# Optimization experiments

Hardware: AMD Instinct MI355X
Metric: run time of the kernel (lower is better)

## Reference

```python
import jax, jax.numpy as jnp
import numpy as np

B, T, I, H, L = 4096, 3, 16, 512, 8  # batch, seq (fixed=3 by fc1), input, hidden, layers


def setup_inputs() -> dict:
    key = jax.random.key(0)
    ks = jax.random.split(key, 12)
    s = 1.0 / np.sqrt(H)  # PyTorch LSTM init scale
    inp = {
        "x": jax.random.normal(ks[0], (B, T, I), dtype=jnp.float32),
        "W_ih0": jax.random.uniform(ks[1], (4 * H, I), jnp.float32, -s, s),
        "W_ih_rest": jax.random.uniform(ks[2], (L - 1, 4 * H, H), jnp.float32, -s, s),
        "W_hh": jax.random.uniform(ks[3], (L, 4 * H, H), jnp.float32, -s, s),
        "b_ih": jax.random.uniform(ks[4], (L, 4 * H), jnp.float32, -s, s),
        "b_hh": jax.random.uniform(ks[5], (L, 4 * H), jnp.float32, -s, s),
        "fc1_w": jax.random.uniform(ks[6], (64, H * T), jnp.float32, -1 / np.sqrt(H * T), 1 / np.sqrt(H * T)),
        "fc1_b": jax.random.uniform(ks[7], (64,), jnp.float32, -1 / np.sqrt(H * T), 1 / np.sqrt(H * T)),
        "fc2_w": jax.random.uniform(ks[8], (3, 64), jnp.float32, -1 / 8.0, 1 / 8.0),
        "fc2_b": jax.random.uniform(ks[9], (3,), jnp.float32, -1 / 8.0, 1 / 8.0),
    }
    return inp


def _lstm_layer(x_tbd, Wih, Whh, bih, bhh):
    # x_tbd: [T, B, D_in] -> [T, B, H]; PyTorch gate order i, f, g, o
    Bsz = x_tbd.shape[1]
    h0 = jnp.zeros((Bsz, H), x_tbd.dtype)
    c0 = jnp.zeros((Bsz, H), x_tbd.dtype)
    # precompute input projections for all timesteps in one matmul
    xg = jnp.einsum('tbd,gd->tbg', x_tbd, Wih) + (bih + bhh)

    def step(carry, xg_t):
        h, c = carry
        gates = xg_t + h @ Whh.T  # [B, 4H]
        i, f, g, o = jnp.split(gates, 4, axis=-1)
        i = jax.nn.sigmoid(i)
        f = jax.nn.sigmoid(f)
        g = jnp.tanh(g)
        o = jax.nn.sigmoid(o)
        c = f * c + i * g
        h = o * jnp.tanh(c)
        return (h, c), h

    _, hs = jax.lax.scan(step, (h0, c0), xg)
    return hs  # [T, B, H]


def reference(x, W_ih0, W_ih_rest, W_hh, b_ih, b_hh, fc1_w, fc1_b, fc2_w, fc2_b):
    h = jnp.transpose(x, (1, 0, 2))  # [T, B, I] (time-major for scan)
    for l in range(L):
        Wih = W_ih0 if l == 0 else W_ih_rest[l - 1]
        h = _lstm_layer(h, Wih, W_hh[l], b_ih[l], b_hh[l])
        # dropout between layers is inference-disabled (eval mode)
    out = jnp.transpose(h, (1, 0, 2)).reshape(x.shape[0], -1)  # [B, T*H]
    out = out @ fc1_w.T + fc1_b
    out = out @ fc2_w.T + fc2_b
    return out
```

## Files before the change

kernel.cpp:

```cpp
#include <hip/hip_runtime.h>
#include <hip/hip_bf16.h>
#include <math.h>


#define BATCH 4096
#define TT 3
#define HH 512
#define LL 8

typedef __attribute__((ext_vector_type(4))) int   i32x4;

#define S_W 0.04419417382f
#define GSCALE   (S_W / 16129.0f)
#define C_SCALE   8192.0f
#define C_INV     (1.0f / 8192.0f)

__device__ inline void gl_lds16(const void* g, void* l) {
    __builtin_amdgcn_global_load_lds(
        (const __attribute__((address_space(1))) void*)g,
        (__attribute__((address_space(3))) void*)l, 16, 0, 0);
}

__device__ inline float fsig(float x) {
    return __builtin_amdgcn_rcpf(1.f + __expf(-x));
}
__device__ inline float ftanh(float x) {
    const float e = __expf(-2.f * __builtin_fabsf(x));
    const float t = (1.f - e) * __builtin_amdgcn_rcpf(1.f + e);
    return __builtin_copysignf(t, x);
}


__global__ __launch_bounds__(256) void prep_w_i8(
    const float* __restrict__ Wihrest, const float* __restrict__ Whh,
    char* __restrict__ WihPh, char* __restrict__ WhhPh)
{
    const int e = blockIdx.x * 256 + threadIdx.x;
    const int mat = e >> 18;
    const int rem = e & 262143;
    const int row = rem >> 7;
    const int k4  = (rem & 127) << 2;
    const float* src; char *dh;
    if (mat < 7) {
        src = Wihrest + (size_t)mat * 1048576;
        dh = WihPh + (size_t)mat * 1048576;
    } else {
        const int l = mat - 7;
        src = Whh + (size_t)l * 1048576;
        dh = WhhPh + (size_t)l * 1048576;
    }
    const int q = row >> 9, j = row & 511;
    const int np = ((j >> 4) << 6) | (q << 4) | (j & 15);
    const int rw = np & 127;
    const int swz = ((rw >> 1) & 3) << 4;
    const size_t off = (size_t)(np >> 7) * 65536 + (size_t)(k4 >> 6) * 8192
                     + (size_t)rw * 64 + ((k4 & 63) ^ swz);
    const float4 v = *(const float4*)(src + (size_t)row * 512 + k4);
    const float inv = 127.0f / S_W;
    int i0 = __float2int_rn(v.x * inv); i0 = i0 > 127 ? 127 : (i0 < -127 ? -127 : i0);
    int i1 = __float2int_rn(v.y * inv); i1 = i1 > 127 ? 127 : (i1 < -127 ? -127 : i1);
    int i2 = __float2int_rn(v.z * inv); i2 = i2 > 127 ? 127 : (i2 < -127 ? -127 : i2);
    int i3 = __float2int_rn(v.w * inv); i3 = i3 > 127 ? 127 : (i3 < -127 ? -127 : i3);
    unsigned hw = (unsigned char)(signed char)i0 | ((unsigned char)(signed char)i1 << 8) |
                  ((unsigned char)(signed char)i2 << 16) | ((unsigned)(unsigned char)(signed char)i3 << 24);
    *(unsigned*)(dh + off) = hw;
}

__global__ __launch_bounds__(256) void prep_w0_i8(
    const float* __restrict__ W0, char* __restrict__ Dh)
{
    const int row = blockIdx.x * 256 + threadIdx.x;
    if (row >= 2048) return;
    const int q = row >> 9, j = row & 511;
    const int np = ((j >> 4) << 6) | (q << 4) | (j & 15);
    const int sl = (np >> 1) & 3;
    const size_t off = (size_t)(np >> 7) * 8192 + (size_t)(np & 127) * 64;
    const float inv = 127.0f / S_W;
    signed char bh[64];
#pragma unroll
    for (int k = 0; k < 16; ++k) {
        int iv = __float2int_rn(W0[(size_t)row * 16 + k] * inv);
        iv = iv > 127 ? 127 : (iv < -127 ? -127 : iv);
        bh[k] = (signed char)iv;
    }
#pragma unroll
    for (int k = 16; k < 64; ++k) bh[k] = 0;
#pragma unroll
    for (int i = 0; i < 4; ++i) {
        *(int4*)(Dh + off + (i ^ sl) * 16) = *(int4*)(bh + i * 16);
    }
}

__global__ __launch_bounds__(256) void prep_x_i8(
    const float* __restrict__ x, char* __restrict__ Xh)
{
    const int id = blockIdx.x * 256 + threadIdx.x;
    if (id >= TT * BATCH) return;
    const int t = id >> 12, b = id & 4095;
    const float* src = x + ((size_t)b * TT + t) * 16;
    const int sl = (b >> 1) & 3;
    const size_t off = (size_t)t * 262144 + (size_t)(b >> 7) * 8192 + (size_t)(b & 127) * 64;
    const float inv = 127.0f / 8.0f;
    signed char bh[64];
#pragma unroll
    for (int k = 0; k < 16; ++k) {
        int iv = __float2int_rn(src[k] * inv);
        iv = iv > 127 ? 127 : (iv < -127 ? -127 : iv);
        bh[k] = (signed char)iv;
    }
#pragma unroll
    for (int k = 16; k < 64; ++k) bh[k] = 0;
#pragma unroll
    for (int i = 0; i < 4; ++i) {
        *(int4*)(Xh + off + (i ^ sl) * 16) = *(int4*)(bh + i * 16);
    }
}

__global__ __launch_bounds__(256) void prep_bsum(
    const float* __restrict__ bih, const float* __restrict__ bhh, float* __restrict__ Bsum)
{
    const int id = blockIdx.x * 256 + threadIdx.x;
    if (id >= LL * 2048) return;
    const int l = id >> 11, row = id & 2047;
    const int q = row >> 9, j = row & 511;
    const int np = ((j >> 4) << 6) | (q << 4) | (j & 15);
    Bsum[(size_t)l * 2048 + np] = bih[(size_t)l * 2048 + row] + bhh[(size_t)l * 2048 + row];
}

__global__ __launch_bounds__(256) void prep_fc1t(
    const float* __restrict__ fc1w, float* __restrict__ fc1T)
{
    const int id = blockIdx.x * 256 + threadIdx.x;
    if (id >= 64 * 1536) return;
    const int m = id / 1536, k = id % 1536;
    fc1T[(size_t)k * 64 + m] = fc1w[id];
}


struct CellDesc {
    const char* A0h;
    const char* W0h;
    const char* A1h;
    const char* W1h;
    const float* bsum; const short* Cin;
    char* HoutH;
    short* Cout; float* Hf32;
    int nk0, aStr0, wStr0, shiftAmt;
};
struct DiagArgs { CellDesc c[3]; };

__global__ __launch_bounds__(512, 8) void lstm_diag(DiagArgs args)
{
    __shared__ char ldsA[2][8192];
    __shared__ char ldsB[3][8192];
    const int tid = threadIdx.x;
    const CellDesc d = args.c[blockIdx.x >> 9];
    const int inner = blockIdx.x & 511;
    const int xcd = inner & 7, q8 = inner >> 3;
    const int mrow = ((xcd & 3) << 3) | (q8 & 7);
    const int col  = ((xcd >> 2) << 3) | (q8 >> 3);
    const int m0 = mrow << 7;
    const int lane = tid & 63, wid = tid >> 6;
    const int wr = wid >> 1;
    const int wc = wid & 1;
    const int ln = lane & 15, lh = lane >> 4;
    const int sl = (ln >> 1) & 3;

    const int nkTot = d.nk0 + (d.A1h ? 8 : 0);
    const int start = (d.shiftAmt == 0) ? (((q8 & 3) * nkTot) >> 2) : 0;

    const int lhs = (lh ^ sl) << 4;
    const int aO0 = (((wr << 5) + (0 << 4) + ln) << 6) + lhs;
    const int aO1 = (((wr << 5) + (1 << 4) + ln) << 6) + lhs;
    const int bO0 = (((wc << 6) + (0 << 4) + ln) << 6) + lhs;
    const int bO1 = (((wc << 6) + (1 << 4) + ln) << 6) + lhs;
    const int bO2 = (((wc << 6) + (2 << 4) + ln) << 6) + lhs;
    const int bO3 = (((wc << 6) + (3 << 4) + ln) << 6) + lhs;

    i32x4 accM[2][4];
#pragma unroll
    for (int m = 0; m < 2; ++m)
#pragma unroll
        for (int n = 0; n < 4; ++n) accM[m][n] = (i32x4){0,0,0,0};

    auto stageA = [&](int ks, int buf) {
        const char *pA;
        if (ks < d.nk0) {
            pA = d.A0h + (size_t)mrow * d.aStr0 + (size_t)ks * 8192;
        } else {
            pA = d.A1h + (size_t)mrow * 65536 + (size_t)(ks - d.nk0) * 8192;
        }
        const int o = tid << 4;
        gl_lds16(pA + o, &ldsA[buf][0] + o);
    };
    auto stageB = [&](int ks, int buf) {
        const char *pB;
        if (ks < d.nk0) {
            pB = d.W0h + (size_t)col * d.wStr0 + (size_t)ks * 8192;
        } else {
            pB = d.W1h + (size_t)col * 65536 + (size_t)(ks - d.nk0) * 8192;
        }
        const int o = tid << 4;
        gl_lds16(pB + o, &ldsB[buf][0] + o);
    };
    auto ksAt = [&](int i) { int k = start + i; return (k >= nkTot) ? k - nkTot : k; };

    stageA(ksAt(0), 0);
    stageB(ksAt(0), 0);
    if (nkTot > 1) {
        stageB(ksAt(1), 1);
        asm volatile("s_waitcnt vmcnt(1)" ::: "memory");
    } else {
        asm volatile("s_waitcnt vmcnt(0)" ::: "memory");
    }
    __builtin_amdgcn_s_barrier();

    int bb = 0;
    for (int i = 0; i < nkTot; ++i) {
        const int ab = i & 1;
        if (i + 1 < nkTot) stageA(ksAt(i + 1), ab ^ 1);
        const bool haveB2 = (i + 2 < nkTot);
        if (haveB2) { int nb = bb + 2; if (nb >= 3) nb -= 3; stageB(ksAt(i + 2), nb); }

        const char* dA = &ldsA[ab][0];
        const char* dB = &ldsB[bb][0];
        i32x4 a_h[2];
        a_h[0] = *(const i32x4*)(dA + aO0);
        a_h[1] = *(const i32x4*)(dA + aO1);
        i32x4 b_0, b_1, b_2, b_3;
        b_0 = *(const i32x4*)(dB + bO0);
        b_1 = *(const i32x4*)(dB + bO1);
        __builtin_amdgcn_s_setprio(1);
#pragma unroll
        for (int m = 0; m < 2; ++m)
            accM[m][0] = __builtin_amdgcn_mfma_i32_16x16x64_i8(a_h[m], b_0, accM[m][0], 0, 0, 0);
        b_2 = *(const i32x4*)(dB + bO2);
#pragma unroll
        for (int m = 0; m < 2; ++m)
            accM[m][1] = __builtin_amdgcn_mfma_i32_16x16x64_i8(a_h[m], b_1, accM[m][1], 0, 0, 0);
        b_3 = *(const i32x4*)(dB + bO3);
#pragma unroll
        for (int m = 0; m < 2; ++m)
            accM[m][2] = __builtin_amdgcn_mfma_i32_16x16x64_i8(a_h[m], b_2, accM[m][2], 0, 0, 0);
#pragma unroll
        for (int m = 0; m < 2; ++m)
            accM[m][3] = __builtin_amdgcn_mfma_i32_16x16x64_i8(a_h[m], b_3, accM[m][3], 0, 0, 0);
        __builtin_amdgcn_s_setprio(0);

        if (d.shiftAmt && ksAt(i) == d.nk0 - 1) {
#pragma unroll
            for (int m = 0; m < 2; ++m)
#pragma unroll
                for (int n = 0; n < 4; ++n)
#pragma unroll
                    for (int r = 0; r < 4; ++r)
                        accM[m][n][r] <<= d.shiftAmt;
        }

        if (haveB2) { asm volatile("s_waitcnt vmcnt(1) lgkmcnt(0)" ::: "memory"); }
        else        { asm volatile("s_waitcnt vmcnt(0) lgkmcnt(0)" ::: "memory"); }
        __builtin_amdgcn_s_barrier();
        ++bb; if (bb >= 3) bb -= 3;
    }

    const int jblk = (col << 1) + wc;
    const int j = (jblk << 4) + ln;
    const int jk = j & 63;
    float bq[4];
#pragma unroll
    for (int g = 0; g < 4; ++g) bq[g] = d.bsum[(jblk << 6) + (g << 4) + ln];
    const size_t hPan = (size_t)mrow * 65536 + (size_t)(j >> 6) * 8192;
#pragma unroll
    for (int m = 0; m < 2; ++m) {
#pragma unroll
        for (int r = 0; r < 4; ++r) {
            const int b = m0 + (wr << 5) + (m << 4) + (lh << 2) + r;
            const float gi = (float)accM[m][0][r] * GSCALE + bq[0];
            const float gf = (float)accM[m][1][r] * GSCALE + bq[1];
            const float gg = (float)accM[m][2][r] * GSCALE + bq[2];
            const float go = (float)accM[m][3][r] * GSCALE + bq[3];
            const float si = fsig(gi);
            const float sf = fsig(gf);
            const float tg = ftanh(gg);
            const float so = fsig(go);
            const size_t ix = (size_t)b * HH + j;
            const float cp = d.Cin ? (float)d.Cin[ix] * C_INV : 0.f;
            const float c = sf * cp + si * tg;
            const float h = so * ftanh(c);
            d.Cout[ix] = (short)__float2int_rn(c * C_SCALE);
            if (d.Hf32) d.Hf32[ix] = h;
            const int ih = __float2int_rn(h * 127.f);
            const int fb = (((lh << 2) + r) >> 1) & 3;
            const size_t ho = hPan + (size_t)(b & 127) * 64 + (size_t)(jk ^ (fb << 4));
            d.HoutH[ho] = (signed char)ih;
        }
    }
}

__global__ __launch_bounds__(256) void fc1_part_f32(
    const float* __restrict__ Hf,
    const float* __restrict__ fc1T, float* __restrict__ midp)
{
    __shared__ float As[32][128];
    __shared__ float Bs[32][64];
    const int tid = threadIdx.x;
    const int b0 = blockIdx.x << 7;
    const int kc = blockIdx.y;
    const int bl = tid & 127, kh = tid >> 7;
    const int mq = tid & 15, rq = tid >> 4;
    float acc[8][4];
#pragma unroll
    for (int r = 0; r < 8; ++r)
#pragma unroll
        for (int c = 0; c < 4; ++c) acc[r][c] = 0.f;

    for (int k0 = 0; k0 < 256; k0 += 32) {
        const int kf = kc * 256 + k0;
        const int tI = kf >> 9, h0 = kf & 511;
        __syncthreads();
        {
            const float* src = Hf + ((size_t)tI * BATCH + b0 + bl) * HH + h0 + (kh << 4);
#pragma unroll
            for (int i = 0; i < 4; ++i) {
                float4 v = *(const float4*)(src + (i << 2));
                As[(kh << 4) + (i << 2) + 0][bl] = v.x;
                As[(kh << 4) + (i << 2) + 1][bl] = v.y;
                As[(kh << 4) + (i << 2) + 2][bl] = v.z;
                As[(kh << 4) + (i << 2) + 3][bl] = v.w;
            }
            const float4* s4 = (const float4*)(fc1T + (size_t)kf * 64);
            float4* d4 = (float4*)(&Bs[0][0]);
            d4[tid] = s4[tid];
            d4[tid + 256] = s4[tid + 256];
        }
        __syncthreads();
#pragma unroll
        for (int kk = 0; kk < 32; ++kk) {
            float a0[4], a1[4], bv[4];
            *(float4*)a0 = *(const float4*)&As[kk][rq << 3];
            *(float4*)a1 = *(const float4*)&As[kk][(rq << 3) + 4];
            *(float4*)bv = *(const float4*)&Bs[kk][mq << 2];
#pragma unroll
            for (int r = 0; r < 4; ++r)
#pragma unroll
                for (int c = 0; c < 4; ++c) {
                    acc[r][c]     += a0[r] * bv[c];
                    acc[r + 4][c] += a1[r] * bv[c];
                }
        }
    }
#pragma unroll
    for (int r = 0; r < 8; ++r) {
        float4 v = make_float4(acc[r][0], acc[r][1], acc[r][2], acc[r][3]);
        *(float4*)(midp + ((size_t)blockIdx.y * BATCH + b0 + (rq << 3) + r) * 64 + (mq << 2)) = v;
    }
}

__global__ __launch_bounds__(256) void fc_red(
    const float* __restrict__ midp, const float* __restrict__ fc1b,
    const float* __restrict__ fc2w, const float* __restrict__ fc2b,
    float* __restrict__ out)
{
    __shared__ float mids[8][64];
    const int tid = threadIdx.x;
    const int b0 = blockIdx.x << 3;
    const int m = tid & 63, rh = tid >> 6;
#pragma unroll
    for (int rr = rh; rr < 8; rr += 4) {
        const int b = b0 + rr;
        float s = fc1b[m];
#pragma unroll
        for (int kc = 0; kc < 6; ++kc) s += midp[((size_t)kc * BATCH + b) * 64 + m];
        mids[rr][m] = s;
    }
    __syncthreads();
    if (tid < 24) {
        const int rr = tid / 3, n = tid % 3;
        float s = fc2b[n];
#pragma unroll
        for (int k = 0; k < 64; ++k) s += mids[rr][k] * fc2w[n * 64 + k];
        out[(size_t)(b0 + rr) * 3 + n] = s;
    }
}

#define BM 64
#define BJ 64
#define KB 32
#define PAD 4

__global__ __launch_bounds__(256) void lstm_cell(
    const float* __restrict__ Xin, int xin_stride, int Din,
    const float* __restrict__ Wih,
    const float* __restrict__ Hprev,
    const float* __restrict__ Whh,
    const float* __restrict__ bih, const float* __restrict__ bhh,
    const float* __restrict__ Cin,
    float* __restrict__ Hout,
    float* __restrict__ Cout)
{
    __shared__ float As2[KB][BM + PAD];
    __shared__ float Bs2[4][KB][BJ + PAD];
    const int tid = threadIdx.x;
    const int row0 = blockIdx.x * BM;
    const int j0 = blockIdx.y * BJ;
    float acc[8][8];
#pragma unroll
    for (int r = 0; r < 8; ++r)
#pragma unroll
        for (int c = 0; c < 8; ++c) acc[r][c] = 0.f;
    const int tr = tid >> 5;
    const int tc = tid & 31;
    const int tc2 = tc * 2;
    for (int ph = 0; ph < 2; ++ph) {
        const float* Ap; const float* Wp;
        int astr, K, wstr;
        if (ph == 0) { Ap = Xin; astr = xin_stride; K = Din; Wp = Wih; wstr = Din; }
        else { if (Hprev == nullptr) break; Ap = Hprev; astr = HH; K = HH; Wp = Whh; wstr = HH; }
        for (int k0 = 0; k0 < K; k0 += KB) {
            int kw = K - k0; if (kw > KB) kw = KB;
            __syncthreads();
            {
                const int k4 = (tid & 7) * 4;
                const int rb = tid >> 3;
#pragma unroll
                for (int it = 0; it < 2; ++it) {
                    const int r = rb + it * 32;
                    float4 v = make_float4(0.f, 0.f, 0.f, 0.f);
                    if (k4 < kw) v = *(const float4*)(Ap + (size_t)(row0 + r) * astr + k0 + k4);
                    As2[k4 + 0][r] = v.x; As2[k4 + 1][r] = v.y; As2[k4 + 2][r] = v.z; As2[k4 + 3][r] = v.w;
                }
            }
            {
                const int k4 = (tid & 7) * 4;
                const int jb = tid >> 3;
#pragma unroll
                for (int q = 0; q < 4; ++q)
#pragma unroll
                    for (int it = 0; it < 2; ++it) {
                        const int jj = jb + it * 32;
                        float4 v = make_float4(0.f, 0.f, 0.f, 0.f);
                        if (k4 < kw) v = *(const float4*)(Wp + (size_t)(q * HH + j0 + jj) * wstr + k0 + k4);
                        Bs2[q][k4 + 0][jj] = v.x; Bs2[q][k4 + 1][jj] = v.y;
                        Bs2[q][k4 + 2][jj] = v.z; Bs2[q][k4 + 3][jj] = v.w;
                    }
            }
            __syncthreads();
#pragma unroll
            for (int k = 0; k < KB; ++k) {
                float a[8];
                *(float4*)(a) = *(const float4*)&As2[k][tr * 8];
                *(float4*)(a + 4) = *(const float4*)&As2[k][tr * 8 + 4];
#pragma unroll
                for (int q = 0; q < 4; ++q) {
                    const float2 bv = *(const float2*)&Bs2[q][k][tc2];
#pragma unroll
                    for (int r = 0; r < 8; ++r) {
                        acc[r][q * 2 + 0] += a[r] * bv.x;
                        acc[r][q * 2 + 1] += a[r] * bv.y;
                    }
                }
            }
        }
    }
#pragma unroll
    for (int jj = 0; jj < 2; ++jj) {
        const int j = j0 + tc2 + jj;
        const float bi_i = bih[0 * HH + j] + bhh[0 * HH + j];
        const float bi_f = bih[1 * HH + j] + bhh[1 * HH + j];
        const float bi_g = bih[2 * HH + j] + bhh[2 * HH + j];
        const float bi_o = bih[3 * HH + j] + bhh[3 * HH + j];
#pragma unroll
        for (int r = 0; r < 8; ++r) {
            const int b = row0 + tr * 8 + r;
            const float gi = acc[r][0 + jj] + bi_i;
            const float gf = acc[r][2 + jj] + bi_f;
            const float gg = acc[r][4 + jj] + bi_g;
            const float go = acc[r][6 + jj] + bi_o;
            const float i_ = 1.f / (1.f + expf(-gi));
            const float f_ = 1.f / (1.f + expf(-gf));
            const float g_ = tanhf(gg);
            const float o_ = 1.f / (1.f + expf(-go));
            const float cp = Cin ? Cin[(size_t)b * HH + j] : 0.f;
            const float c = f_ * cp + i_ * g_;
            const float h = o_ * tanhf(c);
            Hout[(size_t)b * HH + j] = h;
            Cout[(size_t)b * HH + j] = c;
        }
    }
}

__global__ __launch_bounds__(256) void fc_head(
    const float* __restrict__ hfin,
    const float* __restrict__ fc1w, const float* __restrict__ fc1b,
    const float* __restrict__ fc2w, const float* __restrict__ fc2b,
    float* __restrict__ out)
{
    __shared__ float hrow[4][TT * HH];
    __shared__ float mids[4][64 + 1];
    const int tid = threadIdx.x;
    const int b0 = blockIdx.x * 64;
    for (int it = 0; it < 16; ++it) {
        const int rbase = b0 + it * 4;
        __syncthreads();
        for (int v = tid; v < 1536; v += 256) {
            const int r = v / 384;
            const int k4 = v % 384;
            const int k = k4 * 4;
            const int t = k >> 9;
            const int h = k & 511;
            float4 val = *(const float4*)(hfin + ((size_t)t * BATCH + (rbase + r)) * HH + h);
            *(float4*)&hrow[r][k] = val;
        }
        __syncthreads();
        {
            const int m = tid & 63;
            const int r = tid >> 6;
            float s = fc1b[m];
            const float* wrow = fc1w + (size_t)m * (TT * HH);
            for (int k = 0; k < TT * HH; ++k) s += hrow[r][k] * wrow[k];
            mids[r][m] = s;
        }
        __syncthreads();
        if (tid < 12) {
            const int rr = tid / 3, n = tid % 3;
            float s2 = fc2b[n];
#pragma unroll
            for (int mm = 0; mm < 64; ++mm) s2 += mids[rr][mm] * fc2w[n * 64 + mm];
            out[(size_t)(rbase + rr) * 3 + n] = s2;
        }
    }
}


extern "C" void kernel_launch(void* const* d_in, const int* in_sizes, int n_in,
                              void* d_out, int out_size, void* d_ws, size_t ws_size,
                              hipStream_t stream) {
    const float* x        = (const float*)d_in[0];
    const float* W_ih0    = (const float*)d_in[1];
    const float* W_ihrest = (const float*)d_in[2];
    const float* W_hh     = (const float*)d_in[3];
    const float* b_ih     = (const float*)d_in[4];
    const float* b_hh     = (const float*)d_in[5];
    const float* fc1w     = (const float*)d_in[6];
    const float* fc1b     = (const float*)d_in[7];
    const float* fc2w     = (const float*)d_in[8];
    const float* fc2b     = (const float*)d_in[9];

    size_t off = 0;
    char* base = (char*)d_ws;
    auto take = [&](size_t bytes) -> void* {
        void* r = base + off;
        off += (bytes + 255) & ~(size_t)255;
        return r;
    };
    char* WihPh = (char*)take(7UL * 1048576);
    char* WhhPh = (char*)take(8UL * 1048576);
    char* W0Ph  = (char*)take(16UL * 8192);
    char* XPh   = (char*)take(3UL * 262144);
    float* Bsum = (float*)take(8UL * 2048 * 4);
    char *Hh[2];
    Hh[0] = (char*)take(3UL * 2097152);
    Hh[1] = (char*)take(3UL * 2097152);
    short* Cbuf = (short*)take(8UL * 4096 * 512 * 2);
    float* HfBuf = (float*)take(3UL * 4096 * 512 * 4);
    float* Fc1T = (float*)take(1536UL * 64 * 4);
    float* Midp = (float*)take(6UL * 4096 * 64 * 4);
    const size_t need = off;

    if (ws_size < need) {
        float* ws = (float*)d_ws;
        const size_t hsz = (size_t)TT * BATCH * HH;
        float* hb[2] = { ws, ws + hsz };
        float* cb = ws + 2 * hsz;
        dim3 grid(BATCH / BM, HH / BJ), blk(256);
        for (int l = 0; l < LL; ++l) {
            const float* Wih = (l == 0) ? W_ih0 : W_ihrest + (size_t)(l - 1) * 2048 * HH;
            const float* Whh = W_hh + (size_t)l * 2048 * HH;
            const float* bi = b_ih + l * 2048;
            const float* bh = b_hh + l * 2048;
            float* hout_base = hb[l & 1];
            const float* hin_base = hb[(l + 1) & 1];
            for (int t = 0; t < TT; ++t) {
                const float* Xin; int xstr, Din;
                if (l == 0) { Xin = x + t * 16; xstr = TT * 16; Din = 16; }
                else { Xin = hin_base + (size_t)t * BATCH * HH; xstr = HH; Din = HH; }
                const float* Hprev = (t == 0) ? nullptr : hout_base + (size_t)(t - 1) * BATCH * HH;
                const float* Cin = (t == 0) ? nullptr : cb;
                hipLaunchKernelGGL(lstm_cell, grid, blk, 0, stream,
                    Xin, xstr, Din, Wih, Hprev, Whh, bi, bh, Cin,
                    hout_base + (size_t)t * BATCH * HH, cb);
            }
        }
        fc_head<<<dim3(BATCH / 64), blk, 0, stream>>>(hb[1], fc1w, fc1b, fc2w, fc2b, (float*)d_out);
        return;
    }

    prep_w_i8<<<dim3(15360), dim3(256), 0, stream>>>(W_ihrest, W_hh, WihPh, WhhPh);
    prep_w0_i8<<<dim3(8), dim3(256), 0, stream>>>(W_ih0, W0Ph);
    prep_x_i8<<<dim3(48), dim3(256), 0, stream>>>(x, XPh);
    prep_bsum<<<dim3(64), dim3(256), 0, stream>>>(b_ih, b_hh, Bsum);
    prep_fc1t<<<dim3(384), dim3(256), 0, stream>>>(fc1w, Fc1T);

    for (int diag = 0; diag <= (LL - 1) + (TT - 1); ++diag) {
        DiagArgs da;
        int nc = 0;
        for (int t = 0; t < TT; ++t) {
            const int l = diag - t;
            if (l < 0 || l >= LL) continue;
            CellDesc cd;
            if (l == 0) {
                cd.A0h = XPh + (size_t)t * 262144;
                cd.nk0 = 1; cd.aStr0 = 8192;
                cd.W0h = W0Ph; cd.wStr0 = 8192;
                cd.shiftAmt = 3;
            } else {
                cd.A0h = Hh[(l + 1) & 1] + (size_t)t * 2097152;
                cd.nk0 = 8; cd.aStr0 = 65536;
                cd.W0h = WihPh + (size_t)(l - 1) * 1048576;
                cd.wStr0 = 65536;
                cd.shiftAmt = 0;
            }
            cd.A1h = (t == 0) ? nullptr : Hh[l & 1] + (size_t)(t - 1) * 2097152;
            cd.W1h = WhhPh + (size_t)l * 1048576;
            cd.bsum = Bsum + (size_t)l * 2048;
            short* cl = Cbuf + (size_t)l * 2097152;
            cd.Cin = (t == 0) ? nullptr : cl;
            cd.Cout = cl;
            cd.HoutH = Hh[l & 1] + (size_t)t * 2097152;
            cd.Hf32 = (l == LL - 1) ? HfBuf + (size_t)t * 2097152 : nullptr;
            da.c[nc++] = cd;
        }
        if (nc) lstm_diag<<<dim3(512 * nc), dim3(512), 0, stream>>>(da);
    }

    fc1_part_f32<<<dim3(32, 6), dim3(256), 0, stream>>>(HfBuf, Fc1T, Midp);
    fc_red<<<dim3(512), dim3(256), 0, stream>>>(Midp, fc1b, fc2w, fc2b, (float*)d_out);
}
```

Measured before the change: 317.8 us.

## Double the N tile per block in lstm_diag, halving grid size

```diff
diff --git a/kernel.cpp b/kernel.cpp
--- a/kernel.cpp
+++ b/kernel.cpp
@@ -149,20 +149,20 @@
 };
 struct DiagArgs { CellDesc c[3]; };
 
-__global__ __launch_bounds__(512, 8) void lstm_diag(DiagArgs args)
+__global__ __launch_bounds__(512, 4) void lstm_diag(DiagArgs args)
 {
     __shared__ char ldsA[2][8192];
-    __shared__ char ldsB[3][8192];
+    __shared__ char ldsB[3][16384];
     const int tid = threadIdx.x;
-    const CellDesc d = args.c[blockIdx.x >> 9];
-    const int inner = blockIdx.x & 511;
+    const CellDesc d = args.c[blockIdx.x >> 8];
+    const int inner = blockIdx.x & 255;
     const int xcd = inner & 7, q8 = inner >> 3;
     const int mrow = ((xcd & 3) << 3) | (q8 & 7);
-    const int col  = ((xcd >> 2) << 3) | (q8 >> 3);
+    const int col  = ((xcd >> 2) << 2) | (q8 >> 3);
     const int m0 = mrow << 7;
     const int lane = tid & 63, wid = tid >> 6;
-    const int wr = wid >> 1;
-    const int wc = wid & 1;
+    const int wr = wid >> 2;
+    const int wc = wid & 3;
     const int ln = lane & 15, lh = lane >> 4;
     const int sl = (ln >> 1) & 3;
 
@@ -170,18 +170,24 @@
     const int start = (d.shiftAmt == 0) ? (((q8 & 3) * nkTot) >> 2) : 0;
 
     const int lhs = (lh ^ sl) << 4;
-    const int aO0 = (((wr << 5) + (0 << 4) + ln) << 6) + lhs;
-    const int aO1 = (((wr << 5) + (1 << 4) + ln) << 6) + lhs;
-    const int bO0 = (((wc << 6) + (0 << 4) + ln) << 6) + lhs;
-    const int bO1 = (((wc << 6) + (1 << 4) + ln) << 6) + lhs;
-    const int bO2 = (((wc << 6) + (2 << 4) + ln) << 6) + lhs;
-    const int bO3 = (((wc << 6) + (3 << 4) + ln) << 6) + lhs;
-
-    i32x4 accM[2][4];
-#pragma unroll
-    for (int m = 0; m < 2; ++m)
-#pragma unroll
-        for (int n = 0; n < 4; ++n) accM[m][n] = (i32x4){0,0,0,0};
+    const int aO0 = (((wr << 6) + (0 << 4) + ln) << 6) + lhs;
+    const int aO1 = (((wr << 6) + (1 << 4) + ln) << 6) + lhs;
+    const int aO2 = (((wr << 6) + (2 << 4) + ln) << 6) + lhs;
+    const int aO3 = (((wr << 6) + (3 << 4) + ln) << 6) + lhs;
+    const int bnp0 = (wc << 6) + (0 << 4) + ln;
+    const int bnp1 = (wc << 6) + (1 << 4) + ln;
+    const int bnp2 = (wc << 6) + (2 << 4) + ln;
+    const int bnp3 = (wc << 6) + (3 << 4) + ln;
+    const int bO0 = ((bnp0 >> 7) << 13) + ((bnp0 & 127) << 6) + lhs;
+    const int bO1 = ((bnp1 >> 7) << 13) + ((bnp1 & 127) << 6) + lhs;
+    const int bO2 = ((bnp2 >> 7) << 13) + ((bnp2 & 127) << 6) + lhs;
+    const int bO3 = ((bnp3 >> 7) << 13) + ((bnp3 & 127) << 6) + lhs;
+
+    i32x4 acc[4][4];
+#pragma unroll
+    for (int m = 0; m < 4; ++m)
+#pragma unroll
+        for (int n = 0; n < 4; ++n) acc[m][n] = (i32x4){0,0,0,0};
 
     auto stageA = [&](int ks, int buf) {
         const char *pA;
@@ -196,12 +202,14 @@
     auto stageB = [&](int ks, int buf) {
         const char *pB;
         if (ks < d.nk0) {
-            pB = d.W0h + (size_t)col * d.wStr0 + (size_t)ks * 8192;
+            pB = d.W0h + (size_t)(2 * col) * d.wStr0 + (size_t)ks * 8192;
         } else {
-            pB = d.W1h + (size_t)col * 65536 + (size_t)(ks - d.nk0) * 8192;
-        }
+            pB = d.W1h + (size_t)(2 * col) * 65536 + (size_t)(ks - d.nk0) * 8192;
+        }
+        const size_t w2 = (ks < d.nk0) ? (size_t)d.wStr0 : 65536;
         const int o = tid << 4;
-        gl_lds16(pB + o, &ldsB[buf][0] + o);
+        gl_lds16(pB + o,      &ldsB[buf][0] + o);
+        gl_lds16(pB + w2 + o, &ldsB[buf][8192] + o);
     };
     auto ksAt = [&](int i) { int k = start + i; return (k >= nkTot) ? k - nkTot : k; };
 
@@ -209,7 +217,7 @@
     stageB(ksAt(0), 0);
     if (nkTot > 1) {
         stageB(ksAt(1), 1);
-        asm volatile("s_waitcnt vmcnt(1)" ::: "memory");
+        asm volatile("s_waitcnt vmcnt(2)" ::: "memory");
     } else {
         asm volatile("s_waitcnt vmcnt(0)" ::: "memory");
     }
@@ -224,46 +232,51 @@
 
         const char* dA = &ldsA[ab][0];
         const char* dB = &ldsB[bb][0];
-        i32x4 a_h[2];
-        a_h[0] = *(const i32x4*)(dA + aO0);
-        a_h[1] = *(const i32x4*)(dA + aO1);
+        i32x4 a0 = *(const i32x4*)(dA + aO0);
+        i32x4 a1 = *(const i32x4*)(dA + aO1);
+        i32x4 a2 = *(const i32x4*)(dA + aO2);
+        i32x4 a3 = *(const i32x4*)(dA + aO3);
         i32x4 b_0, b_1, b_2, b_3;
         b_0 = *(const i32x4*)(dB + bO0);
         b_1 = *(const i32x4*)(dB + bO1);
         __builtin_amdgcn_s_setprio(1);
-#pragma unroll
-        for (int m = 0; m < 2; ++m)
-            accM[m][0] = __builtin_amdgcn_mfma_i32_16x16x64_i8(a_h[m], b_0, accM[m][0], 0, 0, 0);
+        acc[0][0] = __builtin_amdgcn_mfma_i32_16x16x64_i8(a0, b_0, acc[0][0], 0, 0, 0);
+        acc[1][0] = __builtin_amdgcn_mfma_i32_16x16x64_i8(a1, b_0, acc[1][0], 0, 0, 0);
+        acc[2][0] = __builtin_amdgcn_mfma_i32_16x16x64_i8(a2, b_0, acc[2][0], 0, 0, 0);
+        acc[3][0] = __builtin_amdgcn_mfma_i32_16x16x64_i8(a3, b_0, acc[3][0], 0, 0, 0);
         b_2 = *(const i32x4*)(dB + bO2);
-#pragma unroll
-        for (int m = 0; m < 2; ++m)
-            accM[m][1] = __builtin_amdgcn_mfma_i32_16x16x64_i8(a_h[m], b_1, accM[m][1], 0, 0, 0);
+        acc[0][1] = __builtin_amdgcn_mfma_i32_16x16x64_i8(a0, b_1, acc[0][1], 0, 0, 0);
+        acc[1][1] = __builtin_amdgcn_mfma_i32_16x16x64_i8(a1, b_1, acc[1][1], 0, 0, 0);
+        acc[2][1] = __builtin_amdgcn_mfma_i32_16x16x64_i8(a2, b_1, acc[2][1], 0, 0, 0);
+        acc[3][1] = __builtin_amdgcn_mfma_i32_16x16x64_i8(a3, b_1, acc[3][1], 0, 0, 0);
         b_3 = *(const i32x4*)(dB + bO3);
-#pragma unroll
-        for (int m = 0; m < 2; ++m)
-            accM[m][2] = __builtin_amdgcn_mfma_i32_16x16x64_i8(a_h[m], b_2, accM[m][2], 0, 0, 0);
-#pragma unroll
-        for (int m = 0; m < 2; ++m)
-            accM[m][3] = __builtin_amdgcn_mfma_i32_16x16x64_i8(a_h[m], b_3, accM[m][3], 0, 0, 0);
+        acc[0][2] = __builtin_amdgcn_mfma_i32_16x16x64_i8(a0, b_2, acc[0][2], 0, 0, 0);
+        acc[1][2] = __builtin_amdgcn_mfma_i32_16x16x64_i8(a1, b_2, acc[1][2], 0, 0, 0);
+        acc[2][2] = __builtin_amdgcn_mfma_i32_16x16x64_i8(a2, b_2, acc[2][2], 0, 0, 0);
+        acc[3][2] = __builtin_amdgcn_mfma_i32_16x16x64_i8(a3, b_2, acc[3][2], 0, 0, 0);
+        acc[0][3] = __builtin_amdgcn_mfma_i32_16x16x64_i8(a0, b_3, acc[0][3], 0, 0, 0);
+        acc[1][3] = __builtin_amdgcn_mfma_i32_16x16x64_i8(a1, b_3, acc[1][3], 0, 0, 0);
+        acc[2][3] = __builtin_amdgcn_mfma_i32_16x16x64_i8(a2, b_3, acc[2][3], 0, 0, 0);
+        acc[3][3] = __builtin_amdgcn_mfma_i32_16x16x64_i8(a3, b_3, acc[3][3], 0, 0, 0);
         __builtin_amdgcn_s_setprio(0);
 
         if (d.shiftAmt && ksAt(i) == d.nk0 - 1) {
 #pragma unroll
-            for (int m = 0; m < 2; ++m)
+            for (int m = 0; m < 4; ++m)
 #pragma unroll
                 for (int n = 0; n < 4; ++n)
 #pragma unroll
                     for (int r = 0; r < 4; ++r)
-                        accM[m][n][r] <<= d.shiftAmt;
-        }
-
-        if (haveB2) { asm volatile("s_waitcnt vmcnt(1) lgkmcnt(0)" ::: "memory"); }
+                        acc[m][n][r] <<= d.shiftAmt;
+        }
+
+        if (haveB2) { asm volatile("s_waitcnt vmcnt(2) lgkmcnt(0)" ::: "memory"); }
         else        { asm volatile("s_waitcnt vmcnt(0) lgkmcnt(0)" ::: "memory"); }
         __builtin_amdgcn_s_barrier();
         ++bb; if (bb >= 3) bb -= 3;
     }
 
-    const int jblk = (col << 1) + wc;
+    const int jblk = (col << 2) + wc;
     const int j = (jblk << 4) + ln;
     const int jk = j & 63;
     float bq[4];
@@ -271,14 +284,14 @@
     for (int g = 0; g < 4; ++g) bq[g] = d.bsum[(jblk << 6) + (g << 4) + ln];
     const size_t hPan = (size_t)mrow * 65536 + (size_t)(j >> 6) * 8192;
 #pragma unroll
-    for (int m = 0; m < 2; ++m) {
+    for (int m = 0; m < 4; ++m) {
 #pragma unroll
         for (int r = 0; r < 4; ++r) {
-            const int b = m0 + (wr << 5) + (m << 4) + (lh << 2) + r;
-            const float gi = (float)accM[m][0][r] * GSCALE + bq[0];
-            const float gf = (float)accM[m][1][r] * GSCALE + bq[1];
-            const float gg = (float)accM[m][2][r] * GSCALE + bq[2];
-            const float go = (float)accM[m][3][r] * GSCALE + bq[3];
+            const int b = m0 + (wr << 6) + (m << 4) + (lh << 2) + r;
+            const float gi = (float)acc[m][0][r] * GSCALE + bq[0];
+            const float gf = (float)acc[m][1][r] * GSCALE + bq[1];
+            const float gg = (float)acc[m][2][r] * GSCALE + bq[2];
+            const float go = (float)acc[m][3][r] * GSCALE + bq[3];
             const float si = fsig(gi);
             const float sf = fsig(gf);
             const float tg = ftanh(gg);
@@ -630,7 +643,7 @@
             cd.Hf32 = (l == LL - 1) ? HfBuf + (size_t)t * 2097152 : nullptr;
             da.c[nc++] = cd;
         }
-        if (nc) lstm_diag<<<dim3(512 * nc), dim3(512), 0, stream>>>(da);
+        if (nc) lstm_diag<<<dim3(256 * nc), dim3(512), 0, stream>>>(da);
     }
 
     fc1_part_f32<<<dim3(32, 6), dim3(256), 0, stream>>>(HfBuf, Fc1T, Midp);
```

New measurement: 344.8 us. 1.08x slower.

## Triple-buffer A tiles in LSTM GEMM and merge prep kernels into one launch

Applied to the files above, without the earlier changes.

```diff
diff --git a/kernel.cpp b/kernel.cpp
--- a/kernel.cpp
+++ b/kernel.cpp
@@ -31,109 +31,111 @@
 }
 
 
-__global__ __launch_bounds__(256) void prep_w_i8(
+__global__ __launch_bounds__(256) void prep_all(
     const float* __restrict__ Wihrest, const float* __restrict__ Whh,
-    char* __restrict__ WihPh, char* __restrict__ WhhPh)
+    const float* __restrict__ W0,      const float* __restrict__ x,
+    const float* __restrict__ bih,     const float* __restrict__ bhh,
+    const float* __restrict__ fc1w,
+    char* __restrict__ WihPh, char* __restrict__ WhhPh,
+    char* __restrict__ W0Ph,  char* __restrict__ XPh,
+    float* __restrict__ Bsum, float* __restrict__ fc1T)
 {
-    const int e = blockIdx.x * 256 + threadIdx.x;
-    const int mat = e >> 18;
-    const int rem = e & 262143;
-    const int row = rem >> 7;
-    const int k4  = (rem & 127) << 2;
-    const float* src; char *dh;
-    if (mat < 7) {
-        src = Wihrest + (size_t)mat * 1048576;
-        dh = WihPh + (size_t)mat * 1048576;
-    } else {
-        const int l = mat - 7;
-        src = Whh + (size_t)l * 1048576;
-        dh = WhhPh + (size_t)l * 1048576;
-    }
-    const int q = row >> 9, j = row & 511;
-    const int np = ((j >> 4) << 6) | (q << 4) | (j & 15);
-    const int rw = np & 127;
-    const int swz = ((rw >> 1) & 3) << 4;
-    const size_t off = (size_t)(np >> 7) * 65536 + (size_t)(k4 >> 6) * 8192
-                     + (size_t)rw * 64 + ((k4 & 63) ^ swz);
-    const float4 v = *(const float4*)(src + (size_t)row * 512 + k4);
-    const float inv = 127.0f / S_W;
-    int i0 = __float2int_rn(v.x * inv); i0 = i0 > 127 ? 127 : (i0 < -127 ? -127 : i0);
-    int i1 = __float2int_rn(v.y * inv); i1 = i1 > 127 ? 127 : (i1 < -127 ? -127 : i1);
-    int i2 = __float2int_rn(v.z * inv); i2 = i2 > 127 ? 127 : (i2 < -127 ? -127 : i2);
-    int i3 = __float2int_rn(v.w * inv); i3 = i3 > 127 ? 127 : (i3 < -127 ? -127 : i3);
-    unsigned hw = (unsigned char)(signed char)i0 | ((unsigned char)(signed char)i1 << 8) |
-                  ((unsigned char)(signed char)i2 << 16) | ((unsigned)(unsigned char)(signed char)i3 << 24);
-    *(unsigned*)(dh + off) = hw;
-}
-
-__global__ __launch_bounds__(256) void prep_w0_i8(
-    const float* __restrict__ W0, char* __restrict__ Dh)
-{
-    const int row = blockIdx.x * 256 + threadIdx.x;
-    if (row >= 2048) return;
-    const int q = row >> 9, j = row & 511;
-    const int np = ((j >> 4) << 6) | (q << 4) | (j & 15);
-    const int sl = (np >> 1) & 3;
-    const size_t off = (size_t)(np >> 7) * 8192 + (size_t)(np & 127) * 64;
-    const float inv = 127.0f / S_W;
-    signed char bh[64];
-#pragma unroll
-    for (int k = 0; k < 16; ++k) {
-        int iv = __float2int_rn(W0[(size_t)row * 16 + k] * inv);
-        iv = iv > 127 ? 127 : (iv < -127 ? -127 : iv);
-        bh[k] = (signed char)iv;
-    }
-#pragma unroll
-    for (int k = 16; k < 64; ++k) bh[k] = 0;
-#pragma unroll
-    for (int i = 0; i < 4; ++i) {
-        *(int4*)(Dh + off + (i ^ sl) * 16) = *(int4*)(bh + i * 16);
-    }
-}
-
-__global__ __launch_bounds__(256) void prep_x_i8(
-    const float* __restrict__ x, char* __restrict__ Xh)
-{
-    const int id = blockIdx.x * 256 + threadIdx.x;
-    if (id >= TT * BATCH) return;
-    const int t = id >> 12, b = id & 4095;
-    const float* src = x + ((size_t)b * TT + t) * 16;
-    const int sl = (b >> 1) & 3;
-    const size_t off = (size_t)t * 262144 + (size_t)(b >> 7) * 8192 + (size_t)(b & 127) * 64;
-    const float inv = 127.0f / 8.0f;
-    signed char bh[64];
-#pragma unroll
-    for (int k = 0; k < 16; ++k) {
-        int iv = __float2int_rn(src[k] * inv);
-        iv = iv > 127 ? 127 : (iv < -127 ? -127 : iv);
-        bh[k] = (signed char)iv;
-    }
-#pragma unroll
-    for (int k = 16; k < 64; ++k) bh[k] = 0;
-#pragma unroll
-    for (int i = 0; i < 4; ++i) {
-        *(int4*)(Xh + off + (i ^ sl) * 16) = *(int4*)(bh + i * 16);
-    }
-}
-
-__global__ __launch_bounds__(256) void prep_bsum(
-    const float* __restrict__ bih, const float* __restrict__ bhh, float* __restrict__ Bsum)
-{
-    const int id = blockIdx.x * 256 + threadIdx.x;
-    if (id >= LL * 2048) return;
-    const int l = id >> 11, row = id & 2047;
-    const int q = row >> 9, j = row & 511;
-    const int np = ((j >> 4) << 6) | (q << 4) | (j & 15);
-    Bsum[(size_t)l * 2048 + np] = bih[(size_t)l * 2048 + row] + bhh[(size_t)l * 2048 + row];
-}
-
-__global__ __launch_bounds__(256) void prep_fc1t(
-    const float* __restrict__ fc1w, float* __restrict__ fc1T)
-{
-    const int id = blockIdx.x * 256 + threadIdx.x;
-    if (id >= 64 * 1536) return;
-    const int m = id / 1536, k = id % 1536;
-    fc1T[(size_t)k * 64 + m] = fc1w[id];
+    const int tid = threadIdx.x;
+    int blk = blockIdx.x;
+
+    if (blk < 15360) {
+        const int e = blk * 256 + tid;
+        const int mat = e >> 18;
+        const int rem = e & 262143;
+        const int row = rem >> 7;
+        const int k4  = (rem & 127) << 2;
+        const float* src; char *dh;
+        if (mat < 7) {
+            src = Wihrest + (size_t)mat * 1048576;
+            dh = WihPh + (size_t)mat * 1048576;
+        } else {
+            const int l = mat - 7;
+            src = Whh + (size_t)l * 1048576;
+            dh = WhhPh + (size_t)l * 1048576;
+        }
+        const int q = row >> 9, j = row & 511;
+        const int np = ((j >> 4) << 6) | (q << 4) | (j & 15);
+        const int rw = np & 127;
+        const int swz = ((rw >> 1) & 3) << 4;
+        const size_t off = (size_t)(np >> 7) * 65536 + (size_t)(k4 >> 6) * 8192
+                         + (size_t)rw * 64 + ((k4 & 63) ^ swz);
+        const float4 v = *(const float4*)(src + (size_t)row * 512 + k4);
+        const float inv = 127.0f / S_W;
+        int i0 = __float2int_rn(v.x * inv); i0 = i0 > 127 ? 127 : (i0 < -127 ? -127 : i0);
+        int i1 = __float2int_rn(v.y * inv); i1 = i1 > 127 ? 127 : (i1 < -127 ? -127 : i1);
+        int i2 = __float2int_rn(v.z * inv); i2 = i2 > 127 ? 127 : (i2 < -127 ? -127 : i2);
+        int i3 = __float2int_rn(v.w * inv); i3 = i3 > 127 ? 127 : (i3 < -127 ? -127 : i3);
+        unsigned hw = (unsigned char)(signed char)i0 | ((unsigned char)(signed char)i1 << 8) |
+                      ((unsigned char)(signed char)i2 << 16) | ((unsigned)(unsigned char)(signed char)i3 << 24);
+        *(unsigned*)(dh + off) = hw;
+        return;
+    }
+    blk -= 15360;
+    if (blk < 8) {
+        const int row = blk * 256 + tid;
+        const int q = row >> 9, j = row & 511;
+        const int np = ((j >> 4) << 6) | (q << 4) | (j & 15);
+        const int sl = (np >> 1) & 3;
+        const size_t off = (size_t)(np >> 7) * 8192 + (size_t)(np & 127) * 64;
+        const float inv = 127.0f / S_W;
+        signed char bh[64];
+#pragma unroll
+        for (int k = 0; k < 16; ++k) {
+            int iv = __float2int_rn(W0[(size_t)row * 16 + k] * inv);
+            iv = iv > 127 ? 127 : (iv < -127 ? -127 : iv);
+            bh[k] = (signed char)iv;
+        }
+#pragma unroll
+        for (int k = 16; k < 64; ++k) bh[k] = 0;
+#pragma unroll
+        for (int i = 0; i < 4; ++i) {
+            *(int4*)(W0Ph + off + (i ^ sl) * 16) = *(int4*)(bh + i * 16);
+        }
+        return;
+    }
+    blk -= 8;
+    if (blk < 48) {
+        const int id = blk * 256 + tid;
+        const int t = id >> 12, b = id & 4095;
+        const float* src = x + ((size_t)b * TT + t) * 16;
+        const int sl = (b >> 1) & 3;
+        const size_t off = (size_t)t * 262144 + (size_t)(b >> 7) * 8192 + (size_t)(b & 127) * 64;
+        const float inv = 127.0f / 8.0f;
+        signed char bh[64];
+#pragma unroll
+        for (int k = 0; k < 16; ++k) {
+            int iv = __float2int_rn(src[k] * inv);
+            iv = iv > 127 ? 127 : (iv < -127 ? -127 : iv);
+            bh[k] = (signed char)iv;
+        }
+#pragma unroll
+        for (int k = 16; k < 64; ++k) bh[k] = 0;
+#pragma unroll
+        for (int i = 0; i < 4; ++i) {
+            *(int4*)(XPh + off + (i ^ sl) * 16) = *(int4*)(bh + i * 16);
+        }
+        return;
+    }
+    blk -= 48;
+    if (blk < 64) {
+        const int id = blk * 256 + tid;
+        const int l = id >> 11, row = id & 2047;
+        const int q = row >> 9, j = row & 511;
+        const int np = ((j >> 4) << 6) | (q << 4) | (j & 15);
+        Bsum[(size_t)l * 2048 + np] = bih[(size_t)l * 2048 + row] + bhh[(size_t)l * 2048 + row];
+        return;
+    }
+    blk -= 64;
+    {
+        const int id = blk * 256 + tid;
+        const int m = id / 1536, k = id % 1536;
+        fc1T[(size_t)k * 64 + m] = fc1w[id];
+    }
 }
 
 
@@ -149,9 +151,9 @@
 };
 struct DiagArgs { CellDesc c[3]; };
 
-__global__ __launch_bounds__(512, 8) void lstm_diag(DiagArgs args)
+__global__ __launch_bounds__(512, 6) void lstm_diag(DiagArgs args)
 {
-    __shared__ char ldsA[2][8192];
+    __shared__ char ldsA[3][8192];
     __shared__ char ldsB[3][8192];
     const int tid = threadIdx.x;
     const CellDesc d = args.c[blockIdx.x >> 9];
@@ -208,21 +210,24 @@
     stageA(ksAt(0), 0);
     stageB(ksAt(0), 0);
     if (nkTot > 1) {
+        stageA(ksAt(1), 1);
         stageB(ksAt(1), 1);
-        asm volatile("s_waitcnt vmcnt(1)" ::: "memory");
+        asm volatile("s_waitcnt vmcnt(2)" ::: "memory");
     } else {
         asm volatile("s_waitcnt vmcnt(0)" ::: "memory");
     }
     __builtin_amdgcn_s_barrier();
 
-    int bb = 0;
+    int aa = 0, bb = 0;
     for (int i = 0; i < nkTot; ++i) {
-        const int ab = i & 1;
-        if (i + 1 < nkTot) stageA(ksAt(i + 1), ab ^ 1);
-        const bool haveB2 = (i + 2 < nkTot);
-        if (haveB2) { int nb = bb + 2; if (nb >= 3) nb -= 3; stageB(ksAt(i + 2), nb); }
-
-        const char* dA = &ldsA[ab][0];
+        const bool haveN2 = (i + 2 < nkTot);
+        if (haveN2) {
+            int na = aa + 2; if (na >= 3) na -= 3;
+            stageA(ksAt(i + 2), na);
+            stageB(ksAt(i + 2), na);
+        }
+
+        const char* dA = &ldsA[aa][0];
         const char* dB = &ldsB[bb][0];
         i32x4 a_h[2];
         a_h[0] = *(const i32x4*)(dA + aO0);
@@ -257,9 +262,10 @@
                         accM[m][n][r] <<= d.shiftAmt;
         }
 
-        if (haveB2) { asm volatile("s_waitcnt vmcnt(1) lgkmcnt(0)" ::: "memory"); }
+        if (haveN2) { asm volatile("s_waitcnt vmcnt(2) lgkmcnt(0)" ::: "memory"); }
         else        { asm volatile("s_waitcnt vmcnt(0) lgkmcnt(0)" ::: "memory"); }
         __builtin_amdgcn_s_barrier();
+        ++aa; if (aa >= 3) aa -= 3;
         ++bb; if (bb >= 3) bb -= 3;
     }
 
@@ -595,11 +601,9 @@
         return;
     }
 
-    prep_w_i8<<<dim3(15360), dim3(256), 0, stream>>>(W_ihrest, W_hh, WihPh, WhhPh);
-    prep_w0_i8<<<dim3(8), dim3(256), 0, stream>>>(W_ih0, W0Ph);
-    prep_x_i8<<<dim3(48), dim3(256), 0, stream>>>(x, XPh);
-    prep_bsum<<<dim3(64), dim3(256), 0, stream>>>(b_ih, b_hh, Bsum);
-    prep_fc1t<<<dim3(384), dim3(256), 0, stream>>>(fc1w, Fc1T);
+    prep_all<<<dim3(15360 + 8 + 48 + 64 + 384), dim3(256), 0, stream>>>(
+        W_ihrest, W_hh, W_ih0, x, b_ih, b_hh, fc1w,
+        WihPh, WhhPh, W0Ph, XPh, Bsum, Fc1T);
 
     for (int diag = 0; diag <= (LL - 1) + (TT - 1); ++diag) {
         DiagArgs da;
```

After: 330.7 us. 4.0% more time.
